# Kernel tuning notes

Measured on AMD Instinct MI355X. Metric: run time of the kernel, lower is better.

Reference implementation:

```python
import jax, jax.numpy as jnp
import numpy as np

# --- configuration (matches init_kwargs / input_specs) ---
B = 8            # point clouds per batch
N_PER = 4096     # points per cloud
RATIO = 0.25
M_PER = int(N_PER * RATIO)
K = 64           # max_num_neighbors (hard-coded in source)
R = 0.2          # ball-query radius
C_IN = 64
DIMS = [C_IN + 3, 128, 128, 256]  # local_nn MLP dims (x_j || pos_j - pos_i)


def setup_inputs() -> dict:
    key = jax.random.key(0)
    ks = jax.random.split(key, 8)
    N = B * N_PER
    x = jax.random.normal(ks[0], (N, C_IN), jnp.float32)
    pos = jax.random.uniform(ks[1], (N, 3), jnp.float32)   # unit cube -> r=0.2 meaningful
    batch = jnp.repeat(jnp.arange(B), N_PER)               # sorted cloud ids
    params = {}
    for i, (din, dout) in enumerate(zip(DIMS[:-1], DIMS[1:])):
        params[f"W{i+1}"] = jax.random.normal(ks[2 + i], (din, dout), jnp.float32) / np.sqrt(din)
        params[f"b{i+1}"] = jnp.zeros((dout,), jnp.float32)
    return {"x": x, "pos": pos, "batch": batch, **params}


def _fps(pos, m):
    """Farthest point sampling on one cloud. pos: [n,3] -> [m] int32 indices.
    Deterministic start at index 0 (torch_geometric uses a random start)."""
    n = pos.shape[0]

    def step(carry, _):
        d, cur = carry
        dist = jnp.sum((pos - pos[cur]) ** 2, axis=-1)
        d = jnp.minimum(d, dist)
        nxt = jnp.argmax(d).astype(jnp.int32)
        return (d, nxt), cur

    init = (jnp.full((n,), jnp.inf, pos.dtype), jnp.int32(0))
    (_, _), idx = jax.lax.scan(step, init, None, length=m)
    return idx  # [m]


def _sa_one(x, pos, W1, b1, W2, b2, W3, b3):
    """One cloud: fps -> radius ball query (<=K nearest within R) -> PointConv (max aggr)."""
    idx = _fps(pos, M_PER)                 # [m]
    q = pos[idx]                           # [m,3] centroids
    d2 = jnp.sum((q[:, None, :] - pos[None, :, :]) ** 2, axis=-1)  # [m,n]
    negd, nbr = jax.lax.top_k(-d2, K)      # K nearest candidates per centroid
    valid = (-negd) <= R * R               # inside the radius ball (self always valid)
    rel = pos[nbr] - q[:, None, :]         # [m,K,3]  pos_j - pos_i
    h = jnp.concatenate([x[nbr], rel], axis=-1)   # [m,K,C+3]
    h = jax.nn.relu(h @ W1 + b1)
    h = jax.nn.relu(h @ W2 + b2)
    h = jax.nn.relu(h @ W3 + b3)           # [m,K,256]
    h = jnp.where(valid[..., None], h, -jnp.inf)
    out = jnp.max(h, axis=1)               # max aggregation over neighbors
    out = jnp.where(jnp.any(valid, axis=1)[..., None], out, 0.0)
    return out, idx


def reference(x, pos, batch, W1, b1, W2, b2, W3, b3):
    xb = x.reshape(B, N_PER, C_IN)
    pb = pos.reshape(B, N_PER, 3)
    out, idx = jax.vmap(lambda xc, pc: _sa_one(xc, pc, W1, b1, W2, b2, W3, b3))(xb, pb)
    pos_out = jnp.take_along_axis(pb, idx[..., None], axis=1).reshape(B * M_PER, 3)
    batch_out = jnp.repeat(jnp.arange(B), M_PER)
    return out.reshape(B * M_PER, DIMS[-1]), pos_out, batch_out
```

## Files before the change

### kernel.cpp

```cpp
#include <hip/hip_runtime.h>


#define NB 8
#define NP 4096
#define MP 1024
#define NC 8192
#define CIN 64
#define D1 128
#define D2 128
#define D3 256
#define CAP 512

static constexpr float R2F = 0.04f;

typedef _Float16 f16;
typedef _Float16 half8 __attribute__((ext_vector_type(8)));
typedef float floatx4 __attribute__((ext_vector_type(4)));
typedef unsigned long long u64;

#define OUT1 ((size_t)NC * D3)
#define OUT2 (OUT1 + (size_t)NC * 3)

__global__ void cvt_kernel(const float* __restrict__ W1, const float* __restrict__ W2,
                           const float* __restrict__ W3, f16* __restrict__ W2t,
                           f16* __restrict__ W3t, float* __restrict__ W1b) {
  const int stride = gridDim.x * blockDim.x;
  const int i = blockIdx.x * blockDim.x + threadIdx.x;
  for (int e = i; e < D1 * D2; e += stride) {
    int c = e >> 7, k = e & 127;
    W2t[c * 128 + k] = (f16)W2[k * D2 + c];
  }
  for (int e = i; e < D2 * D3; e += stride) {
    int c = e >> 7, k = e & 127;
    W3t[c * 128 + k] = (f16)W3[k * D3 + c];
  }
  for (int e = i; e < 3 * D1; e += stride) W1b[e] = W1[64 * D1 + e];
}

__launch_bounds__(256)
__global__ void pk_kernel(const float* __restrict__ x, const float* __restrict__ W1,
                          const float* __restrict__ b1, f16* __restrict__ P) {
  __shared__ float wl[CIN * D1];
  __shared__ float xl[32 * CIN];
  const int t = threadIdx.x;
  const int r0 = blockIdx.x * 32;
  for (int e = t; e < CIN * D1; e += 256) wl[e] = W1[e];
  for (int e = t; e < 32 * CIN; e += 256)
    xl[e] = x[(size_t)(r0 + (e >> 6)) * CIN + (e & 63)];
  __syncthreads();
  const int c = t & 127;
  const int rh = t >> 7;
  const float bc = b1[c];
  for (int rr = 0; rr < 32; rr += 2) {
    const int r = rr + rh;
    float acc = bc;
    #pragma unroll
    for (int k = 0; k < CIN; ++k) acc = __fmaf_rn(xl[r * CIN + k], wl[k * D1 + c], acc);
    P[(size_t)(r0 + r) * D1 + c] = (f16)acc;
  }
}

template<int CTRL>
__device__ __forceinline__ float dppmax(float v) {
  const int iv = __builtin_bit_cast(int, v);
  const int sh = __builtin_amdgcn_update_dpp(iv, iv, CTRL, 0xf, 0xf, false);
  return fmaxf(v, __builtin_bit_cast(float, sh));
}

__launch_bounds__(256)
__global__ void fps_kernel(const float* __restrict__ pos, float* __restrict__ qpos,
                           float* __restrict__ dout) {
  __shared__ float ldspos[NP * 3];
  __shared__ u64 pkey[2][4];
  __shared__ int cidx[MP];
  const int b = blockIdx.x;
  const int t = threadIdx.x;
  const int lane = t & 63, wv = t >> 6;
  for (int e = t; e < NP * 3; e += 256) ldspos[e] = pos[(size_t)b * NP * 3 + e];
  __syncthreads();
  float px[16], py[16], pz[16], d[16];
  #pragma unroll
  for (int i = 0; i < 16; ++i) {
    const int p = t * 16 + i;
    px[i] = ldspos[p * 3 + 0]; py[i] = ldspos[p * 3 + 1]; pz[i] = ldspos[p * 3 + 2];
    d[i] = INFINITY;
  }
  int g = 0;
  for (int step = 0; step < MP; ++step) {
    if (t == 0) cidx[step] = g;
    const float cx = ldspos[g * 3 + 0], cy = ldspos[g * 3 + 1], cz = ldspos[g * 3 + 2];
    float lv = -1.0f;
    #pragma unroll
    for (int i = 0; i < 16; ++i) {
      const float dx = __fsub_rn(px[i], cx);
      const float dy = __fsub_rn(py[i], cy);
      const float dz = __fsub_rn(pz[i], cz);
      const float nd = __fadd_rn(__fadd_rn(__fmul_rn(dx, dx), __fmul_rn(dy, dy)),
                                 __fmul_rn(dz, dz));
      d[i] = fminf(d[i], nd);
      lv = fmaxf(lv, d[i]);
    }
    int li = 15;
    #pragma unroll
    for (int i = 14; i >= 0; --i) li = (d[i] == lv) ? i : li;
    float wm = lv;
    wm = dppmax<0xB1>(wm);
    wm = dppmax<0x4E>(wm);
    wm = dppmax<0x141>(wm);
    wm = dppmax<0x140>(wm);
    wm = dppmax<0x142>(wm);
    wm = dppmax<0x143>(wm);
    const float M = __builtin_bit_cast(float,
        __builtin_amdgcn_readlane(__builtin_bit_cast(int, wm), 63));
    const u64 bal = __ballot(lv == M);
    const int Ls = (int)__builtin_ctzll(bal);
    const int sli = __builtin_amdgcn_readlane(li, Ls);
    const int gw = ((wv << 6) + Ls) * 16 + sli;
    if (lane == 0)
      pkey[step & 1][wv] = ((u64)__float_as_uint(M) << 32) | (unsigned int)~gw;
    __syncthreads();
    u64 best = pkey[step & 1][0];
    #pragma unroll
    for (int w = 1; w < 4; ++w) {
      const u64 o = pkey[step & 1][w];
      best = o > best ? o : best;
    }
    g = (int)~(unsigned int)best;
  }
  __syncthreads();
  for (int s = t; s < MP; s += 256) {
    const int ci = (b << 10) + s;
    const int p = cidx[s];
    const float cx = ldspos[p * 3 + 0], cy = ldspos[p * 3 + 1], cz = ldspos[p * 3 + 2];
    qpos[ci * 3 + 0] = cx; qpos[ci * 3 + 1] = cy; qpos[ci * 3 + 2] = cz;
    dout[OUT1 + (size_t)ci * 3 + 0] = cx;
    dout[OUT1 + (size_t)ci * 3 + 1] = cy;
    dout[OUT1 + (size_t)ci * 3 + 2] = cz;
    dout[OUT2 + ci] = (float)b;
  }
}

__launch_bounds__(256)
__global__ void ballq_kernel(const float* __restrict__ pos, const float* __restrict__ qpos,
                             int* __restrict__ nbr) {
  __shared__ unsigned long long list[4][CAP];
  const int t = threadIdx.x;
  const int wv = t >> 6, lane = t & 63;
  const int ci = blockIdx.x * 4 + wv;
  const int b = ci >> 10;
  const int base = b * NP;
  const float qx = qpos[ci * 3 + 0], qy = qpos[ci * 3 + 1], qz = qpos[ci * 3 + 2];
  int cnt = 0;
  for (int chunk = 0; chunk < NP / 64; ++chunk) {
    const int p = chunk * 64 + lane;
    const float x = pos[(size_t)(base + p) * 3 + 0];
    const float y = pos[(size_t)(base + p) * 3 + 1];
    const float z = pos[(size_t)(base + p) * 3 + 2];
    const float dx = __fsub_rn(qx, x), dy = __fsub_rn(qy, y), dz = __fsub_rn(qz, z);
    const float d2 = __fadd_rn(__fadd_rn(__fmul_rn(dx, dx), __fmul_rn(dy, dy)),
                               __fmul_rn(dz, dz));
    const bool in = d2 <= R2F;
    const unsigned long long mask = __ballot(in);
    if (in) {
      const int slot = cnt + __popcll(mask & ((1ull << lane) - 1ull));
      if (slot < CAP)
        list[wv][slot] = ((unsigned long long)__float_as_uint(d2) << 32) | (unsigned int)p;
    }
    cnt += __popcll(mask);
  }
  const int cntc = cnt < CAP ? cnt : CAP;
  for (int s = cntc + lane; s < CAP; s += 64) list[wv][s] = ~0ull;
  __syncthreads();
  for (int ks = 2; ks <= CAP; ks <<= 1) {
    for (int jj = ks >> 1; jj > 0; jj >>= 1) {
      for (int i = lane; i < CAP; i += 64) {
        const int partner = i ^ jj;
        if (partner > i) {
          const bool up = ((i & ks) == 0);
          const unsigned long long a = list[wv][i], c = list[wv][partner];
          if (up ? (a > c) : (a < c)) { list[wv][i] = c; list[wv][partner] = a; }
        }
      }
      __syncthreads();
    }
  }
  const unsigned long long e = list[wv][lane];
  const int idx = (int)(e & 0xFFFFFFFFull);
  nbr[(ci << 6) + lane] = (lane < cntc) ? idx : -1;
}

__launch_bounds__(256)
__global__ void mlp_kernel(const float* __restrict__ pos, const float* __restrict__ qpos,
                           const int* __restrict__ nbr, const f16* __restrict__ P,
                           const float* __restrict__ W1b, const f16* __restrict__ W2t,
                           const float* __restrict__ b2c, const f16* __restrict__ W3t,
                           const float* __restrict__ b3c, float* __restrict__ out) {
  __shared__ f16 h1s[64 * 128];
  __shared__ f16 h2s[64 * 128];
  const int ci = blockIdx.x;
  const int base = (ci >> 10) << 12;
  const int t = threadIdx.x;
  const int lane = t & 63;
  const int wv = __builtin_amdgcn_readfirstlane((int)(t >> 6));
  const int m = lane & 15, qq = lane >> 4;

  const int j = nbr[(ci << 6) + lane];
  const bool valid = j >= 0;
  const int cnt = __popcll(__ballot(valid));
  const int j0 = __shfl(j, 0);
  const int jjn = valid ? j : (j0 >= 0 ? j0 : 0);

  const float qx = qpos[ci * 3 + 0], qy = qpos[ci * 3 + 1], qz = qpos[ci * 3 + 2];
  const float rx = pos[(size_t)(base + jjn) * 3 + 0] - qx;
  const float ry = pos[(size_t)(base + jjn) * 3 + 1] - qy;
  const float rz = pos[(size_t)(base + jjn) * 3 + 2] - qz;

  {
    const f16* Prow = P + (size_t)(base + jjn) * D1;
    const int r = lane;
    #pragma unroll
    for (int c8 = 0; c8 < 4; ++c8) {
      const int c0 = wv * 32 + c8 * 8;
      const half8 pv = *(const half8*)(Prow + c0);
      half8 hv;
      #pragma unroll
      for (int u = 0; u < 8; ++u) {
        const int c = c0 + u;
        float v = (float)pv[u] + rx * W1b[c] + ry * W1b[128 + c] + rz * W1b[256 + c];
        hv[u] = (f16)fmaxf(v, 0.0f);
      }
      *(half8*)(h1s + r * 128 + (c0 ^ ((r & 7) << 3))) = hv;
    }
  }
  __syncthreads();

  {
    floatx4 acc[2][4];
    #pragma unroll
    for (int cs = 0; cs < 2; ++cs)
      #pragma unroll
      for (int rt = 0; rt < 4; ++rt) acc[cs][rt] = floatx4{0.f, 0.f, 0.f, 0.f};
    #pragma unroll
    for (int ks = 0; ks < 4; ++ks) {
      const int kk = ks * 32 + qq * 8;
      half8 af[4];
      #pragma unroll
      for (int rt = 0; rt < 4; ++rt) {
        const int r = rt * 16 + m;
        af[rt] = *(const half8*)(h1s + r * 128 + (kk ^ ((r & 7) << 3)));
      }
      half8 bf[2];
      #pragma unroll
      for (int cs = 0; cs < 2; ++cs) {
        const int c = (wv * 2 + cs) * 16 + m;
        bf[cs] = *(const half8*)(W2t + (size_t)c * 128 + kk);
      }
      #pragma unroll
      for (int cs = 0; cs < 2; ++cs)
        #pragma unroll
        for (int rt = 0; rt < 4; ++rt)
          acc[cs][rt] = __builtin_amdgcn_mfma_f32_16x16x32_f16(af[rt], bf[cs], acc[cs][rt], 0, 0, 0);
    }
    #pragma unroll
    for (int cs = 0; cs < 2; ++cs) {
      const int c = (wv * 2 + cs) * 16 + m;
      const float bias = b2c[c];
      #pragma unroll
      for (int rt = 0; rt < 4; ++rt) {
        #pragma unroll
        for (int u = 0; u < 4; ++u) {
          const int r = rt * 16 + qq * 4 + u;
          h2s[r * 128 + (c ^ ((r & 7) << 3))] = (f16)fmaxf(acc[cs][rt][u] + bias, 0.0f);
        }
      }
    }
  }
  __syncthreads();

  {
    floatx4 acc[4][4];
    #pragma unroll
    for (int ct = 0; ct < 4; ++ct)
      #pragma unroll
      for (int rt = 0; rt < 4; ++rt) acc[ct][rt] = floatx4{0.f, 0.f, 0.f, 0.f};
    #pragma unroll
    for (int ks = 0; ks < 4; ++ks) {
      const int kk = ks * 32 + qq * 8;
      half8 af[4];
      #pragma unroll
      for (int rt = 0; rt < 4; ++rt) {
        const int r = rt * 16 + m;
        af[rt] = *(const half8*)(h2s + r * 128 + (kk ^ ((r & 7) << 3)));
      }
      half8 bf[4];
      #pragma unroll
      for (int ct = 0; ct < 4; ++ct) {
        const int c = (wv * 4 + ct) * 16 + m;
        bf[ct] = *(const half8*)(W3t + (size_t)c * 128 + kk);
      }
      #pragma unroll
      for (int ct = 0; ct < 4; ++ct)
        #pragma unroll
        for (int rt = 0; rt < 4; ++rt)
          acc[ct][rt] = __builtin_amdgcn_mfma_f32_16x16x32_f16(af[rt], bf[ct], acc[ct][rt], 0, 0, 0);
    }
    #pragma unroll
    for (int ct = 0; ct < 4; ++ct) {
      const int c = (wv * 4 + ct) * 16 + m;
      const float bias = b3c[c];
      float mx = -INFINITY;
      #pragma unroll
      for (int rt = 0; rt < 4; ++rt) {
        #pragma unroll
        for (int u = 0; u < 4; ++u) {
          const int r = rt * 16 + qq * 4 + u;
          float v = fmaxf(acc[ct][rt][u] + bias, 0.0f);
          v = (r < cnt) ? v : -INFINITY;
          mx = fmaxf(mx, v);
        }
      }
      mx = fmaxf(mx, __shfl_xor(mx, 16));
      mx = fmaxf(mx, __shfl_xor(mx, 32));
      mx = (cnt > 0) ? mx : 0.0f;
      if (qq == 0) out[(size_t)ci * D3 + c] = mx;
    }
  }
}

extern "C" void kernel_launch(void* const* d_in, const int* in_sizes, int n_in,
                              void* d_out, int out_size, void* d_ws, size_t ws_size,
                              hipStream_t stream) {
  const float* x   = (const float*)d_in[0];
  const float* pos = (const float*)d_in[1];
  const float* W1 = (const float*)d_in[3];
  const float* b1 = (const float*)d_in[4];
  const float* W2 = (const float*)d_in[5];
  const float* b2 = (const float*)d_in[6];
  const float* W3 = (const float*)d_in[7];
  const float* b3 = (const float*)d_in[8];
  float* out = (float*)d_out;

  char* ws = (char*)d_ws;
  f16*   P    = (f16*)  (ws + 0);
  float* qpos = (float*)(ws + 8388608);
  int*   nbr  = (int*)  (ws + 8486912);
  f16*   W2t  = (f16*)  (ws + 10584064);
  f16*   W3t  = (f16*)  (ws + 10616832);
  float* W1b  = (float*)(ws + 10682368);

  cvt_kernel<<<64, 256, 0, stream>>>(W1, W2, W3, W2t, W3t, W1b);
  pk_kernel<<<NB * NP / 32, 256, 0, stream>>>(x, W1, b1, P);
  fps_kernel<<<NB, 256, 0, stream>>>(pos, qpos, out);
  ballq_kernel<<<NC / 4, 256, 0, stream>>>(pos, qpos, nbr);
  mlp_kernel<<<NC, 256, 0, stream>>>(pos, qpos, nbr, P, W1b, W2t, b2, W3t, b3, out);
}
```

Baseline: 875.8 us.

## Replace per-step FPS barrier with LDS flag polling and packed-float distance math

In the farthest-point-sampling loop, the per-step __syncthreads and double-buffered key slots are replaced by a per-step key array of MP x 4 slots. Each wave writes its key with a volatile store and spins until all four slots are nonzero, which removes the block-wide barrier from the serial critical path. The per-point distance update is also rewritten on two-wide float vectors so the compiler can emit packed FP32 ops, with fp contraction disabled to keep the rounding the same. The cost is 32 KB of extra LDS, which lowers occupancy (only one block per cloud runs anyway), and it relies on volatile LDS ordering between waves.

```diff
diff --git a/kernel.cpp b/kernel.cpp
--- a/kernel.cpp
+++ b/kernel.cpp
@@ -16,6 +16,7 @@
 typedef _Float16 f16;
 typedef _Float16 half8 __attribute__((ext_vector_type(8)));
 typedef float floatx4 __attribute__((ext_vector_type(4)));
+typedef float f32x2 __attribute__((ext_vector_type(2)));
 typedef unsigned long long u64;
 
 #define OUT1 ((size_t)NC * D3)
@@ -70,39 +71,47 @@
 __launch_bounds__(256)
 __global__ void fps_kernel(const float* __restrict__ pos, float* __restrict__ qpos,
                            float* __restrict__ dout) {
+  #pragma clang fp contract(off)
   __shared__ float ldspos[NP * 3];
-  __shared__ u64 pkey[2][4];
+  __shared__ u64 pkey[MP][4];
   __shared__ int cidx[MP];
   const int b = blockIdx.x;
   const int t = threadIdx.x;
   const int lane = t & 63, wv = t >> 6;
+  for (int e = t; e < MP * 4; e += 256) ((u64*)pkey)[e] = 0ull;
   for (int e = t; e < NP * 3; e += 256) ldspos[e] = pos[(size_t)b * NP * 3 + e];
   __syncthreads();
-  float px[16], py[16], pz[16], d[16];
+  f32x2 px[8], py[8], pz[8], dv[8];
   #pragma unroll
-  for (int i = 0; i < 16; ++i) {
-    const int p = t * 16 + i;
-    px[i] = ldspos[p * 3 + 0]; py[i] = ldspos[p * 3 + 1]; pz[i] = ldspos[p * 3 + 2];
-    d[i] = INFINITY;
+  for (int i = 0; i < 8; ++i) {
+    const int p = t * 16 + 2 * i;
+    px[i] = (f32x2){ldspos[p * 3 + 0], ldspos[p * 3 + 3]};
+    py[i] = (f32x2){ldspos[p * 3 + 1], ldspos[p * 3 + 4]};
+    pz[i] = (f32x2){ldspos[p * 3 + 2], ldspos[p * 3 + 5]};
+    dv[i] = INFINITY;
   }
   int g = 0;
   for (int step = 0; step < MP; ++step) {
     if (t == 0) cidx[step] = g;
     const float cx = ldspos[g * 3 + 0], cy = ldspos[g * 3 + 1], cz = ldspos[g * 3 + 2];
-    float lv = -1.0f;
-    #pragma unroll
-    for (int i = 0; i < 16; ++i) {
-      const float dx = __fsub_rn(px[i], cx);
-      const float dy = __fsub_rn(py[i], cy);
-      const float dz = __fsub_rn(pz[i], cz);
-      const float nd = __fadd_rn(__fadd_rn(__fmul_rn(dx, dx), __fmul_rn(dy, dy)),
-                                 __fmul_rn(dz, dz));
-      d[i] = fminf(d[i], nd);
-      lv = fmaxf(lv, d[i]);
-    }
+    const f32x2 cx2 = cx, cy2 = cy, cz2 = cz;
+    f32x2 lvv = -1.0f;
+    #pragma unroll
+    for (int i = 0; i < 8; ++i) {
+      const f32x2 dx = px[i] - cx2;
+      const f32x2 dy = py[i] - cy2;
+      const f32x2 dz = pz[i] - cz2;
+      const f32x2 nd = (dx * dx + dy * dy) + dz * dz;
+      dv[i] = __builtin_elementwise_min(dv[i], nd);
+      lvv = __builtin_elementwise_max(lvv, dv[i]);
+    }
+    const float lv = fmaxf(lvv.x, lvv.y);
     int li = 15;
     #pragma unroll
-    for (int i = 14; i >= 0; --i) li = (d[i] == lv) ? i : li;
+    for (int i = 14; i >= 0; --i) {
+      const float di = (i & 1) ? dv[i >> 1].y : dv[i >> 1].x;
+      li = (di == lv) ? i : li;
+    }
     float wm = lv;
     wm = dppmax<0xB1>(wm);
     wm = dppmax<0x4E>(wm);
@@ -117,15 +126,16 @@
     const int sli = __builtin_amdgcn_readlane(li, Ls);
     const int gw = ((wv << 6) + Ls) * 16 + sli;
     if (lane == 0)
-      pkey[step & 1][wv] = ((u64)__float_as_uint(M) << 32) | (unsigned int)~gw;
-    __syncthreads();
-    u64 best = pkey[step & 1][0];
-    #pragma unroll
-    for (int w = 1; w < 4; ++w) {
-      const u64 o = pkey[step & 1][w];
-      best = o > best ? o : best;
-    }
-    g = (int)~(unsigned int)best;
+      *(volatile u64*)&pkey[step][wv] =
+          ((u64)__float_as_uint(M) << 32) | (unsigned int)~gw;
+    volatile const u64* pk = &pkey[step][0];
+    u64 k0, k1, k2, k3;
+    do { k0 = pk[0]; k1 = pk[1]; k2 = pk[2]; k3 = pk[3]; }
+    while (k0 == 0ull || k1 == 0ull || k2 == 0ull || k3 == 0ull);
+    u64 ba = k0 > k1 ? k0 : k1;
+    const u64 bb = k2 > k3 ? k2 : k3;
+    ba = ba > bb ? ba : bb;
+    g = (int)~(unsigned int)ba;
   }
   __syncthreads();
   for (int s = t; s < MP; s += 256) {
```

Measured after the change: 986.0 us. 1.13x slower.

## Fuse FPS, layer-1 projection and weight conversion into one concurrent front kernel

Applied to the files above, without the earlier changes.

Combines the farthest-point-sampling kernel, the per-point layer-1 projection kernel and the weight transpose/convert kernel into one launch, with blocks dispatched by block index to each role. The eight long serial FPS blocks can then run concurrently with the projection and conversion blocks instead of waiting behind them on the stream, and two launches are removed. The risk is that all blocks now reserve the larger FPS shared-memory size and share the register allocation of the heaviest branch, which may lower occupancy for the projection blocks.

```diff
diff --git a/kernel.cpp b/kernel.cpp
--- a/kernel.cpp
+++ b/kernel.cpp
@@ -21,45 +21,6 @@
 #define OUT1 ((size_t)NC * D3)
 #define OUT2 (OUT1 + (size_t)NC * 3)
 
-__global__ void cvt_kernel(const float* __restrict__ W1, const float* __restrict__ W2,
-                           const float* __restrict__ W3, f16* __restrict__ W2t,
-                           f16* __restrict__ W3t, float* __restrict__ W1b) {
-  const int stride = gridDim.x * blockDim.x;
-  const int i = blockIdx.x * blockDim.x + threadIdx.x;
-  for (int e = i; e < D1 * D2; e += stride) {
-    int c = e >> 7, k = e & 127;
-    W2t[c * 128 + k] = (f16)W2[k * D2 + c];
-  }
-  for (int e = i; e < D2 * D3; e += stride) {
-    int c = e >> 7, k = e & 127;
-    W3t[c * 128 + k] = (f16)W3[k * D3 + c];
-  }
-  for (int e = i; e < 3 * D1; e += stride) W1b[e] = W1[64 * D1 + e];
-}
-
-__launch_bounds__(256)
-__global__ void pk_kernel(const float* __restrict__ x, const float* __restrict__ W1,
-                          const float* __restrict__ b1, f16* __restrict__ P) {
-  __shared__ float wl[CIN * D1];
-  __shared__ float xl[32 * CIN];
-  const int t = threadIdx.x;
-  const int r0 = blockIdx.x * 32;
-  for (int e = t; e < CIN * D1; e += 256) wl[e] = W1[e];
-  for (int e = t; e < 32 * CIN; e += 256)
-    xl[e] = x[(size_t)(r0 + (e >> 6)) * CIN + (e & 63)];
-  __syncthreads();
-  const int c = t & 127;
-  const int rh = t >> 7;
-  const float bc = b1[c];
-  for (int rr = 0; rr < 32; rr += 2) {
-    const int r = rr + rh;
-    float acc = bc;
-    #pragma unroll
-    for (int k = 0; k < CIN; ++k) acc = __fmaf_rn(xl[r * CIN + k], wl[k * D1 + c], acc);
-    P[(size_t)(r0 + r) * D1 + c] = (f16)acc;
-  }
-}
-
 template<int CTRL>
 __device__ __forceinline__ float dppmax(float v) {
   const int iv = __builtin_bit_cast(int, v);
@@ -67,76 +28,115 @@
   return fmaxf(v, __builtin_bit_cast(float, sh));
 }
 
+struct FpsS { float ldspos[NP * 3]; u64 pkey[2][4]; int cidx[MP]; };
+struct PkS  { float wl[CIN * D1]; float xl[32 * CIN]; };
+
 __launch_bounds__(256)
-__global__ void fps_kernel(const float* __restrict__ pos, float* __restrict__ qpos,
-                           float* __restrict__ dout) {
-  __shared__ float ldspos[NP * 3];
-  __shared__ u64 pkey[2][4];
-  __shared__ int cidx[MP];
-  const int b = blockIdx.x;
+__global__ void front_kernel(const float* __restrict__ pos, const float* __restrict__ x,
+                             const float* __restrict__ W1, const float* __restrict__ b1,
+                             const float* __restrict__ W2, const float* __restrict__ W3,
+                             float* __restrict__ qpos, f16* __restrict__ P,
+                             f16* __restrict__ W2t, f16* __restrict__ W3t,
+                             float* __restrict__ W1b, float* __restrict__ dout) {
+  __shared__ __align__(16) char raw[sizeof(FpsS)];
+  const int bid = blockIdx.x;
   const int t = threadIdx.x;
-  const int lane = t & 63, wv = t >> 6;
-  for (int e = t; e < NP * 3; e += 256) ldspos[e] = pos[(size_t)b * NP * 3 + e];
-  __syncthreads();
-  float px[16], py[16], pz[16], d[16];
-  #pragma unroll
-  for (int i = 0; i < 16; ++i) {
-    const int p = t * 16 + i;
-    px[i] = ldspos[p * 3 + 0]; py[i] = ldspos[p * 3 + 1]; pz[i] = ldspos[p * 3 + 2];
-    d[i] = INFINITY;
-  }
-  int g = 0;
-  for (int step = 0; step < MP; ++step) {
-    if (t == 0) cidx[step] = g;
-    const float cx = ldspos[g * 3 + 0], cy = ldspos[g * 3 + 1], cz = ldspos[g * 3 + 2];
-    float lv = -1.0f;
+
+  if (bid < NB) {
+    FpsS& S = *reinterpret_cast<FpsS*>(raw);
+    const int b = bid;
+    const int lane = t & 63, wv = t >> 6;
+    for (int e = t; e < NP * 3; e += 256) S.ldspos[e] = pos[(size_t)b * NP * 3 + e];
+    __syncthreads();
+    float px[16], py[16], pz[16], d[16];
     #pragma unroll
     for (int i = 0; i < 16; ++i) {
-      const float dx = __fsub_rn(px[i], cx);
-      const float dy = __fsub_rn(py[i], cy);
-      const float dz = __fsub_rn(pz[i], cz);
-      const float nd = __fadd_rn(__fadd_rn(__fmul_rn(dx, dx), __fmul_rn(dy, dy)),
-                                 __fmul_rn(dz, dz));
-      d[i] = fminf(d[i], nd);
-      lv = fmaxf(lv, d[i]);
-    }
-    int li = 15;
-    #pragma unroll
-    for (int i = 14; i >= 0; --i) li = (d[i] == lv) ? i : li;
-    float wm = lv;
-    wm = dppmax<0xB1>(wm);
-    wm = dppmax<0x4E>(wm);
-    wm = dppmax<0x141>(wm);
-    wm = dppmax<0x140>(wm);
-    wm = dppmax<0x142>(wm);
-    wm = dppmax<0x143>(wm);
-    const float M = __builtin_bit_cast(float,
-        __builtin_amdgcn_readlane(__builtin_bit_cast(int, wm), 63));
-    const u64 bal = __ballot(lv == M);
-    const int Ls = (int)__builtin_ctzll(bal);
-    const int sli = __builtin_amdgcn_readlane(li, Ls);
-    const int gw = ((wv << 6) + Ls) * 16 + sli;
-    if (lane == 0)
-      pkey[step & 1][wv] = ((u64)__float_as_uint(M) << 32) | (unsigned int)~gw;
+      const int p = t * 16 + i;
+      px[i] = S.ldspos[p * 3 + 0]; py[i] = S.ldspos[p * 3 + 1]; pz[i] = S.ldspos[p * 3 + 2];
+      d[i] = INFINITY;
+    }
+    int g = 0;
+    for (int step = 0; step < MP; ++step) {
+      if (t == 0) S.cidx[step] = g;
+      const float cx = S.ldspos[g * 3 + 0], cy = S.ldspos[g * 3 + 1], cz = S.ldspos[g * 3 + 2];
+      float lv = -1.0f;
+      #pragma unroll
+      for (int i = 0; i < 16; ++i) {
+        const float dx = __fsub_rn(px[i], cx);
+        const float dy = __fsub_rn(py[i], cy);
+        const float dz = __fsub_rn(pz[i], cz);
+        const float nd = __fadd_rn(__fadd_rn(__fmul_rn(dx, dx), __fmul_rn(dy, dy)),
+                                   __fmul_rn(dz, dz));
+        d[i] = fminf(d[i], nd);
+        lv = fmaxf(lv, d[i]);
+      }
+      int li = 15;
+      #pragma unroll
+      for (int i = 14; i >= 0; --i) li = (d[i] == lv) ? i : li;
+      float wm = lv;
+      wm = dppmax<0xB1>(wm);
+      wm = dppmax<0x4E>(wm);
+      wm = dppmax<0x141>(wm);
+      wm = dppmax<0x140>(wm);
+      wm = dppmax<0x142>(wm);
+      wm = dppmax<0x143>(wm);
+      const float M = __builtin_bit_cast(float,
+          __builtin_amdgcn_readlane(__builtin_bit_cast(int, wm), 63));
+      const u64 bal = __ballot(lv == M);
+      const int Ls = (int)__builtin_ctzll(bal);
+      const int sli = __builtin_amdgcn_readlane(li, Ls);
+      const int gw = ((wv << 6) + Ls) * 16 + sli;
+      if (lane == 0)
+        S.pkey[step & 1][wv] = ((u64)__float_as_uint(M) << 32) | (unsigned int)~gw;
+      __syncthreads();
+      u64 best = S.pkey[step & 1][0];
+      #pragma unroll
+      for (int w = 1; w < 4; ++w) {
+        const u64 o = S.pkey[step & 1][w];
+        best = o > best ? o : best;
+      }
+      g = (int)~(unsigned int)best;
+    }
     __syncthreads();
-    u64 best = pkey[step & 1][0];
-    #pragma unroll
-    for (int w = 1; w < 4; ++w) {
-      const u64 o = pkey[step & 1][w];
-      best = o > best ? o : best;
-    }
-    g = (int)~(unsigned int)best;
-  }
-  __syncthreads();
-  for (int s = t; s < MP; s += 256) {
-    const int ci = (b << 10) + s;
-    const int p = cidx[s];
-    const float cx = ldspos[p * 3 + 0], cy = ldspos[p * 3 + 1], cz = ldspos[p * 3 + 2];
-    qpos[ci * 3 + 0] = cx; qpos[ci * 3 + 1] = cy; qpos[ci * 3 + 2] = cz;
-    dout[OUT1 + (size_t)ci * 3 + 0] = cx;
-    dout[OUT1 + (size_t)ci * 3 + 1] = cy;
-    dout[OUT1 + (size_t)ci * 3 + 2] = cz;
-    dout[OUT2 + ci] = (float)b;
+    for (int s = t; s < MP; s += 256) {
+      const int ci = (b << 10) + s;
+      const int p = S.cidx[s];
+      const float cx = S.ldspos[p * 3 + 0], cy = S.ldspos[p * 3 + 1], cz = S.ldspos[p * 3 + 2];
+      qpos[ci * 3 + 0] = cx; qpos[ci * 3 + 1] = cy; qpos[ci * 3 + 2] = cz;
+      dout[OUT1 + (size_t)ci * 3 + 0] = cx;
+      dout[OUT1 + (size_t)ci * 3 + 1] = cy;
+      dout[OUT1 + (size_t)ci * 3 + 2] = cz;
+      dout[OUT2 + ci] = (float)b;
+    }
+  } else if (bid < NB + 1024) {
+    PkS& S = *reinterpret_cast<PkS*>(raw);
+    const int r0 = (bid - NB) * 32;
+    for (int e = t; e < CIN * D1; e += 256) S.wl[e] = W1[e];
+    for (int e = t; e < 32 * CIN; e += 256)
+      S.xl[e] = x[(size_t)(r0 + (e >> 6)) * CIN + (e & 63)];
+    __syncthreads();
+    const int c = t & 127;
+    const int rh = t >> 7;
+    const float bc = b1[c];
+    for (int rr = 0; rr < 32; rr += 2) {
+      const int r = rr + rh;
+      float acc = bc;
+      #pragma unroll
+      for (int k = 0; k < CIN; ++k) acc = __fmaf_rn(S.xl[r * CIN + k], S.wl[k * D1 + c], acc);
+      P[(size_t)(r0 + r) * D1 + c] = (f16)acc;
+    }
+  } else {
+    const int stride = 64 * 256;
+    const int i = (bid - (NB + 1024)) * 256 + t;
+    for (int e = i; e < D1 * D2; e += stride) {
+      int c = e >> 7, k = e & 127;
+      W2t[c * 128 + k] = (f16)W2[k * D2 + c];
+    }
+    for (int e = i; e < D2 * D3; e += stride) {
+      int c = e >> 7, k = e & 127;
+      W3t[c * 128 + k] = (f16)W3[k * D3 + c];
+    }
+    for (int e = i; e < 3 * D1; e += stride) W1b[e] = W1[64 * D1 + e];
   }
 }
 
@@ -348,9 +348,8 @@
   f16*   W3t  = (f16*)  (ws + 10616832);
   float* W1b  = (float*)(ws + 10682368);
 
-  cvt_kernel<<<64, 256, 0, stream>>>(W1, W2, W3, W2t, W3t, W1b);
-  pk_kernel<<<NB * NP / 32, 256, 0, stream>>>(x, W1, b1, P);
-  fps_kernel<<<NB, 256, 0, stream>>>(pos, qpos, out);
+  front_kernel<<<NB + 1024 + 64, 256, 0, stream>>>(pos, x, W1, b1, W2, W3,
+                                                   qpos, P, W2t, W3t, W1b, out);
   ballq_kernel<<<NC / 4, 256, 0, stream>>>(pos, qpos, nbr);
   mlp_kernel<<<NC, 256, 0, stream>>>(pos, qpos, nbr, P, W1b, W2t, b2, W3t, b3, out);
 }
```

Result: no change. 860.5 us (-1.7%).
